# Kernel optimization log

Measured on AMD Instinct MI355X. Metric: run time of the kernel, lower is better.

Reference implementation:

```python
import jax, jax.numpy as jnp
import numpy as np

PATCHES_PER_INDEX = 50  # config.patches_per_index


def setup_inputs() -> dict:
    key = jax.random.key(0)
    k1, k2, k3 = jax.random.split(key, 3)
    B, L, D = 64, 550, 768
    R = 3  # random_indexes
    x = jax.random.normal(k1, (B, L, D), dtype=jnp.float32)
    noise = jax.random.uniform(k2, (B, L), dtype=jnp.float32)
    indexes = jax.random.randint(k3, (B, R), 0, 11)
    return {"x": x, "noise": noise, "indexes": indexes}


def reference(x, noise, indexes):
    B, L, D = x.shape
    p = PATCHES_PER_INDEX
    R = indexes.shape[1]
    len_keep = L - R * p
    # vectorized scatter replacing the triple Python loop:
    # noise[bi, index*p + i] = 2 for each batch row / masked index / patch offset
    pos = (indexes[:, :, None] * p + jnp.arange(p)).reshape(B, R * p)  # [B, R*p]
    b_idx = jnp.arange(B)[:, None]
    noise = noise.at[b_idx, pos].set(2.0)
    ids_shuffle = jnp.argsort(noise, axis=1)            # [B, L]
    ids_restore = jnp.argsort(ids_shuffle, axis=1)      # [B, L]
    ids_keep = ids_shuffle[:, :len_keep]                # [B, len_keep]
    x_masked = jnp.take_along_axis(x, ids_keep[:, :, None], axis=1)  # [B, len_keep, D]
    mask = jnp.ones((B, L), dtype=x.dtype).at[:, :len_keep].set(0.0)
    mask = jnp.take_along_axis(mask, ids_restore, axis=1)
    return x_masked, mask, ids_restore
```

## Files before the change

### kernel.cpp

```cpp
#include <hip/hip_runtime.h>

#define BB 64
#define LL 550
#define DD 768
#define RR 3
#define PP 50
#define LEN_KEEP 400

#define O_MASK     (BB * LEN_KEEP * DD)
#define O_RESTORE  (O_MASK + BB * LL)

__global__ __launch_bounds__(576) void rank_kernel(
    const float* __restrict__ noise,
    const int*   __restrict__ indexes,
    float*       __restrict__ out,
    int*         __restrict__ ws_rank)
{
    __shared__ float s_noise[LL];
    const int b = blockIdx.x;
    const int t = threadIdx.x;

    if (t < LL) s_noise[t] = noise[b * LL + t];
    __syncthreads();

    if (t < RR * PP) {
        const int r   = t / PP;
        const int idx = indexes[b * RR + r];
        s_noise[idx * PP + (t % PP)] = 2.0f;
    }
    __syncthreads();

    if (t < LL) {
        const float v = s_noise[t];
        int rank = 0;
        #pragma unroll 10
        for (int j = 0; j < LL; ++j) {
            const float vj = s_noise[j];
            rank += (vj < v) || (vj == v && j < t);
        }
        out[O_MASK    + b * LL + t] = (rank >= LEN_KEEP) ? 1.0f : 0.0f;
        out[O_RESTORE + b * LL + t] = (float)rank;
        ws_rank[b * LL + t] = rank;
    }
}

__global__ __launch_bounds__(DD / 4) void gather_kernel(
    const float* __restrict__ x,
    const int*   __restrict__ ws_rank,
    float*       __restrict__ out)
{
    const int i = blockIdx.x;
    const int b = blockIdx.y;
    const int r = ws_rank[b * LL + i];
    if (r >= LEN_KEEP) return;

    const float4* __restrict__ src =
        (const float4*)(x + ((size_t)b * LL + i) * DD);
    float4* __restrict__ dst =
        (float4*)(out + ((size_t)b * LEN_KEEP + r) * DD);
    dst[threadIdx.x] = src[threadIdx.x];
}

extern "C" void kernel_launch(void* const* d_in, const int* in_sizes, int n_in,
                              void* d_out, int out_size, void* d_ws, size_t ws_size,
                              hipStream_t stream)
{
    const float* x       = (const float*)d_in[0];
    const float* noise   = (const float*)d_in[1];
    const int*   indexes = (const int*)  d_in[2];
    float*       out     = (float*)d_out;
    int*         ws_rank = (int*)d_ws;

    rank_kernel<<<BB, 576, 0, stream>>>(noise, indexes, out, ws_rank);

    dim3 grid(LL, BB);
    gather_kernel<<<grid, DD / 4, 0, stream>>>(x, ws_rank, out);
}
```

Measured before the change: 198.0 us.

## Split rank computation across chunks and gather via inverse permutation

The rank kernel now runs three blocks of 192 threads per batch row instead of one 576-thread block, and reads shared-memory noise as float4 with the array padded by sentinel values. It writes an inverse map from kept rank to source row, so the gather kernel launches only the 400 kept rows per batch instead of 550 blocks that mostly exit early. The intent is more parallelism in the ranking pass and fewer wasted gather blocks, at the cost of reloading noise redundantly in each chunk block.

```diff
diff --git a/kernel.cpp b/kernel.cpp
--- a/kernel.cpp
+++ b/kernel.cpp
@@ -6,58 +6,67 @@
 #define RR 3
 #define PP 50
 #define LEN_KEEP 400
+#define CHUNK 192
+#define NCHUNK 3
+#define L4 138
 
 #define O_MASK     (BB * LEN_KEEP * DD)
 #define O_RESTORE  (O_MASK + BB * LL)
 
-__global__ __launch_bounds__(576) void rank_kernel(
+__global__ __launch_bounds__(CHUNK) void rank_kernel(
     const float* __restrict__ noise,
     const int*   __restrict__ indexes,
     float*       __restrict__ out,
-    int*         __restrict__ ws_rank)
+    int*         __restrict__ src_of)
 {
-    __shared__ float s_noise[LL];
-    const int b = blockIdx.x;
+    __shared__ __align__(16) float s_noise[L4 * 4];
+    const int b = blockIdx.y;
+    const int c = blockIdx.x;
     const int t = threadIdx.x;
 
-    if (t < LL) s_noise[t] = noise[b * LL + t];
+    for (int j = t; j < LL; j += CHUNK) s_noise[j] = noise[b * LL + j];
+    if (t < L4 * 4 - LL) s_noise[LL + t] = 1e30f;
     __syncthreads();
 
     if (t < RR * PP) {
-        const int r   = t / PP;
-        const int idx = indexes[b * RR + r];
+        const int idx = indexes[b * RR + t / PP];
         s_noise[idx * PP + (t % PP)] = 2.0f;
     }
     __syncthreads();
 
-    if (t < LL) {
-        const float v = s_noise[t];
+    const int i = c * CHUNK + t;
+    if (i < LL) {
+        const float v = s_noise[i];
+        const float4* __restrict__ s4 = (const float4*)s_noise;
         int rank = 0;
-        #pragma unroll 10
-        for (int j = 0; j < LL; ++j) {
-            const float vj = s_noise[j];
-            rank += (vj < v) || (vj == v && j < t);
+        #pragma unroll 6
+        for (int j4 = 0; j4 < L4; ++j4) {
+            const float4 f = s4[j4];
+            const int j = j4 * 4;
+            rank += (f.x < v) || (f.x == v && (j + 0) < i);
+            rank += (f.y < v) || (f.y == v && (j + 1) < i);
+            rank += (f.z < v) || (f.z == v && (j + 2) < i);
+            rank += (f.w < v) || (f.w == v && (j + 3) < i);
         }
-        out[O_MASK    + b * LL + t] = (rank >= LEN_KEEP) ? 1.0f : 0.0f;
-        out[O_RESTORE + b * LL + t] = (float)rank;
-        ws_rank[b * LL + t] = rank;
+        out[O_MASK    + b * LL + i] = (rank >= LEN_KEEP) ? 1.0f : 0.0f;
+        out[O_RESTORE + b * LL + i] = (float)rank;
+        if (rank < LEN_KEEP) src_of[b * LEN_KEEP + rank] = i;
     }
 }
 
 __global__ __launch_bounds__(DD / 4) void gather_kernel(
     const float* __restrict__ x,
-    const int*   __restrict__ ws_rank,
+    const int*   __restrict__ src_of,
     float*       __restrict__ out)
 {
-    const int i = blockIdx.x;
+    const int d = blockIdx.x;
     const int b = blockIdx.y;
-    const int r = ws_rank[b * LL + i];
-    if (r >= LEN_KEEP) return;
+    const int i = src_of[b * LEN_KEEP + d];
 
     const float4* __restrict__ src =
         (const float4*)(x + ((size_t)b * LL + i) * DD);
     float4* __restrict__ dst =
-        (float4*)(out + ((size_t)b * LEN_KEEP + r) * DD);
+        (float4*)(out + ((size_t)b * LEN_KEEP + d) * DD);
     dst[threadIdx.x] = src[threadIdx.x];
 }
 
@@ -69,10 +78,11 @@
     const float* noise   = (const float*)d_in[1];
     const int*   indexes = (const int*)  d_in[2];
     float*       out     = (float*)d_out;
-    int*         ws_rank = (int*)d_ws;
+    int*         src_of  = (int*)d_ws;
 
-    rank_kernel<<<BB, 576, 0, stream>>>(noise, indexes, out, ws_rank);
+    dim3 rgrid(NCHUNK, BB);
+    rank_kernel<<<rgrid, CHUNK, 0, stream>>>(noise, indexes, out, src_of);
 
-    dim3 grid(LL, BB);
-    gather_kernel<<<grid, DD / 4, 0, stream>>>(x, ws_rank, out);
+    dim3 ggrid(LEN_KEEP, BB);
+    gather_kernel<<<ggrid, DD / 4, 0, stream>>>(x, src_of, out);
 }
```

Result: faster. 193.6 us (-2.2%).
